# Performance work log

Hardware: AMD Instinct MI355X
Metric: run time of the kernel (lower is better)

## Reference

```python
import jax, jax.numpy as jnp
import numpy as np

N, D, L = 524288, 64, 20  # tokens, in_features, chain depth (20 Linear layers per branch)


def setup_inputs() -> dict:
    key = jax.random.key(0)
    kx, kw, kb = jax.random.split(key, 3)
    x = jax.random.normal(kx, (N, D), dtype=jnp.float32)
    # torch.nn.Linear default init: U(-1/sqrt(fan_in), 1/sqrt(fan_in))
    bound = 1.0 / np.sqrt(D)
    W = jax.random.uniform(kw, (L, D, D), dtype=jnp.float32, minval=-bound, maxval=bound)
    b = jax.random.uniform(kb, (L, D), dtype=jnp.float32, minval=-bound, maxval=bound)
    return {"x": x, "W": W, "b": b}


def reference(x, W, b):
    # is_hit=False => scatter routes ALL tokens to path 1 (path 0 is empty),
    # so forward = branches[1]: 20 sequential Linear(D, D) layers, then a
    # trivial gather (concat of the single non-empty branch result).
    # torch Linear: y = x @ W^T + b, W has shape [out, in].
    def step(h, wb):
        w, bias = wb  # w: [D, D], bias: [D]
        return h @ w.T + bias, None

    out, _ = jax.lax.scan(step, x, (W, b))
    return out
```

## Files before the change

kernel.cpp:

```cpp
#include <hip/hip_runtime.h>
#include <stdint.h>


using short8  = __attribute__((ext_vector_type(8))) short;
using floatx4 = __attribute__((ext_vector_type(4))) float;

#define N_TOK   524288
#define N_LAYER 20

#ifdef __has_builtin
#if __has_builtin(__builtin_amdgcn_cvt_pk_bf16_f32)
#define HAVE_CVT_PK_BF16 1
#endif
#endif

#ifdef HAVE_CVT_PK_BF16
typedef __bf16 bf16x2_t __attribute__((ext_vector_type(2)));
__device__ __forceinline__ uint32_t pk_bf16(float lo, float hi) {
  union { bf16x2_t v; uint32_t u; } c;
  c.v = __builtin_amdgcn_cvt_pk_bf16_f32(lo, hi);
  return c.u;
}
#else
__device__ __forceinline__ uint32_t pk_bf16(float lo, float hi) {
  uint32_t a = __float_as_uint(lo) + 0x8000u;
  uint32_t b = __float_as_uint(hi) + 0x8000u;
  return __builtin_amdgcn_perm(b, a, 0x07060302u);
}
#endif

__device__ __forceinline__ uint16_t bf16_rne(float f) {
  uint32_t u = __float_as_uint(f);
  u += 0x7fffu + ((u >> 16) & 1u);
  return (uint16_t)(u >> 16);
}

__global__ void prep_weights(const float* __restrict__ W, uint16_t* __restrict__ ws) {
  int idx  = blockIdx.x * 256 + threadIdx.x;
  int l    = idx >> 9;
  int rem  = idx & 511;
  int frag = rem >> 6;
  int lane = rem & 63;
  int mt = frag >> 1, ks = frag & 1;
  int m  = lane & 15;
  int q  = lane >> 4;
  int wrow = 32 * (mt >> 1) + 8 * (m >> 2) + 4 * (mt & 1) + (m & 3);
  int k0   = 32 * ks + 8 * q;
  const float* src = W + l * 4096 + wrow * 64 + k0;
  float4 f0 = *(const float4*)(src);
  float4 f1 = *(const float4*)(src + 4);
  union { uint16_t s[8]; uint4 v; } o;
  o.s[0] = bf16_rne(f0.x); o.s[1] = bf16_rne(f0.y);
  o.s[2] = bf16_rne(f0.z); o.s[3] = bf16_rne(f0.w);
  o.s[4] = bf16_rne(f1.x); o.s[5] = bf16_rne(f1.y);
  o.s[6] = bf16_rne(f1.z); o.s[7] = bf16_rne(f1.w);
  *(uint4*)(ws + (size_t)idx * 8) = o.v;
}

union BFrag { short8 v; uint32_t u[4]; };
union AFrag { short8 v; uint4 raw; };

__global__ __launch_bounds__(256, 3) void chain_fused(
    const float* __restrict__ x, const uint16_t* __restrict__ wf,
    const float* __restrict__ bias, float* __restrict__ out)
{
  __shared__ __align__(16) float biasLds[N_LAYER * 64];

  const int tid  = threadIdx.x;
  const int wv   = tid >> 6;
  const int lane = tid & 63;
  const int tl   = lane & 15;
  const int q    = lane >> 4;
  const int tokbase = blockIdx.x * 256 + wv * 64;

  for (int i = tid; i < N_LAYER * 64; i += 256) biasLds[i] = bias[i];

  BFrag Bf[4][2];
  #pragma unroll
  for (int tb = 0; tb < 4; tb++) {
    const float* xp = x + (size_t)(tokbase + tb * 16 + tl) * 64 + 8 * q;
    #pragma unroll
    for (int ks = 0; ks < 2; ks++) {
      float4 a0 = *(const float4*)(xp + 32 * ks);
      float4 a1 = *(const float4*)(xp + 32 * ks + 4);
      Bf[tb][ks].u[0] = pk_bf16(a0.x, a0.y);
      Bf[tb][ks].u[1] = pk_bf16(a0.z, a0.w);
      Bf[tb][ks].u[2] = pk_bf16(a1.x, a1.y);
      Bf[tb][ks].u[3] = pk_bf16(a1.z, a1.w);
    }
  }

  const uint4* wp = (const uint4*)wf;
  AFrag Af[8];
  #pragma unroll
  for (int f = 0; f < 8; f++) Af[f].raw = wp[f * 64 + lane];

  __syncthreads();

  floatx4 acc[4][4];
  #pragma unroll 2
  for (int l = 0; l < N_LAYER; l++) {
    const int ln = (l + 1 < N_LAYER) ? l + 1 : N_LAYER - 1;
    uint4 nf[8];
    #pragma unroll
    for (int f = 0; f < 8; f++) nf[f] = wp[(ln * 8 + f) * 64 + lane];

    #pragma unroll
    for (int mt = 0; mt < 4; mt++) {
      floatx4 bv = *(const floatx4*)(biasLds + l * 64 + 32 * (mt >> 1) + 4 * (mt & 1) + 8 * q);
      #pragma unroll
      for (int tb = 0; tb < 4; tb++) acc[tb][mt] = bv;
    }

    #pragma unroll
    for (int ks = 0; ks < 2; ks++)
      #pragma unroll
      for (int mt = 0; mt < 4; mt++)
        #pragma unroll
        for (int tb = 0; tb < 4; tb++)
          acc[tb][mt] = __builtin_amdgcn_mfma_f32_16x16x32_bf16(
              Af[mt * 2 + ks].v, Bf[tb][ks].v, acc[tb][mt], 0, 0, 0);

    if (l == N_LAYER - 1) break;

    #pragma unroll
    for (int tb = 0; tb < 4; tb++)
      #pragma unroll
      for (int mt = 0; mt < 4; mt++) {
        const int ksn = mt >> 1;
        const int d   = 2 * (mt & 1);
        Bf[tb][ksn].u[d]     = pk_bf16(acc[tb][mt][0], acc[tb][mt][1]);
        Bf[tb][ksn].u[d + 1] = pk_bf16(acc[tb][mt][2], acc[tb][mt][3]);
      }

    #pragma unroll
    for (int f = 0; f < 8; f++) Af[f].raw = nf[f];
  }

  #pragma unroll
  for (int tb = 0; tb < 4; tb++) {
    float* op = out + (size_t)(tokbase + tb * 16 + tl) * 64;
    #pragma unroll
    for (int mt = 0; mt < 4; mt++)
      *(floatx4*)(op + 32 * (mt >> 1) + 4 * (mt & 1) + 8 * q) = acc[tb][mt];
  }
}

extern "C" void kernel_launch(void* const* d_in, const int* in_sizes, int n_in,
                              void* d_out, int out_size, void* d_ws, size_t ws_size,
                              hipStream_t stream) {
  (void)in_sizes; (void)n_in; (void)out_size; (void)ws_size;
  const float* x = (const float*)d_in[0];
  const float* W = (const float*)d_in[1];
  const float* b = (const float*)d_in[2];
  float* out = (float*)d_out;
  uint16_t* ws = (uint16_t*)d_ws;

  prep_weights<<<dim3(40), dim3(256), 0, stream>>>(W, ws);
  chain_fused<<<dim3(N_TOK / 256), dim3(256), 0, stream>>>(x, ws, b, out);
}
```

Baseline: 277.8 us.

## Collapse 20-layer linear chain into a single composed affine map

```diff
diff --git a/kernel.cpp b/kernel.cpp
--- a/kernel.cpp
+++ b/kernel.cpp
@@ -7,6 +7,7 @@
 
 #define N_TOK   524288
 #define N_LAYER 20
+#define FPERM(mt, m) (32 * ((mt) >> 1) + 8 * ((m) >> 2) + 4 * ((mt) & 1) + ((m) & 3))
 
 #ifdef __has_builtin
 #if __has_builtin(__builtin_amdgcn_cvt_pk_bf16_f32)
@@ -29,43 +30,150 @@
 }
 #endif
 
+__device__ __forceinline__ float upk_lo(uint32_t p) { return __uint_as_float(p << 16); }
+__device__ __forceinline__ float upk_hi(uint32_t p) { return __uint_as_float(p & 0xffff0000u); }
+
 __device__ __forceinline__ uint16_t bf16_rne(float f) {
   uint32_t u = __float_as_uint(f);
   u += 0x7fffu + ((u >> 16) & 1u);
   return (uint16_t)(u >> 16);
 }
 
-__global__ void prep_weights(const float* __restrict__ W, uint16_t* __restrict__ ws) {
-  int idx  = blockIdx.x * 256 + threadIdx.x;
-  int l    = idx >> 9;
-  int rem  = idx & 511;
-  int frag = rem >> 6;
-  int lane = rem & 63;
-  int mt = frag >> 1, ks = frag & 1;
-  int m  = lane & 15;
-  int q  = lane >> 4;
-  int wrow = 32 * (mt >> 1) + 8 * (m >> 2) + 4 * (mt & 1) + (m & 3);
-  int k0   = 32 * ks + 8 * q;
-  const float* src = W + l * 4096 + wrow * 64 + k0;
-  float4 f0 = *(const float4*)(src);
-  float4 f1 = *(const float4*)(src + 4);
-  union { uint16_t s[8]; uint4 v; } o;
-  o.s[0] = bf16_rne(f0.x); o.s[1] = bf16_rne(f0.y);
-  o.s[2] = bf16_rne(f0.z); o.s[3] = bf16_rne(f0.w);
-  o.s[4] = bf16_rne(f1.x); o.s[5] = bf16_rne(f1.y);
-  o.s[6] = bf16_rne(f1.z); o.s[7] = bf16_rne(f1.w);
-  *(uint4*)(ws + (size_t)idx * 8) = o.v;
-}
-
 union BFrag { short8 v; uint32_t u[4]; };
-union AFrag { short8 v; uint4 raw; };
-
-__global__ __launch_bounds__(256, 3) void chain_fused(
-    const float* __restrict__ x, const uint16_t* __restrict__ wf,
-    const float* __restrict__ bias, float* __restrict__ out)
+union AFrag { short8 v; uint32_t u[4]; uint4 raw; };
+
+__global__ __launch_bounds__(128, 1) void compose(
+    const float* __restrict__ W, const float* __restrict__ bias,
+    uint16_t* __restrict__ afrag, float* __restrict__ vout)
 {
-  __shared__ __align__(16) float biasLds[N_LAYER * 64];
-
+  __shared__ float comp[65][64];
+
+  const int tid  = threadIdx.x;
+  const int twv  = tid >> 6;
+  const int lane = tid & 63;
+  const int tl   = lane & 15;
+  const int q    = lane >> 4;
+
+  BFrag Bh[4][2], Bl[4][2];
+  #pragma unroll
+  for (int tb = 0; tb < 4; tb++) {
+    const int tok = twv * 64 + tb * 16 + tl;
+    #pragma unroll
+    for (int ks = 0; ks < 2; ks++)
+      #pragma unroll
+      for (int p = 0; p < 4; p++) {
+        const int f0 = 32 * ks + 8 * q + 2 * p;
+        Bh[tb][ks].u[p] = pk_bf16(tok == f0 ? 1.0f : 0.0f, tok == f0 + 1 ? 1.0f : 0.0f);
+        Bl[tb][ks].u[p] = 0u;
+      }
+  }
+
+  floatx4 wr[2][8][2];
+  floatx4 br[2][4];
+
+  #define FETCH(L, buf)                                                          \
+    {                                                                            \
+      _Pragma("unroll") for (int mt = 0; mt < 4; mt++) {                         \
+        const int r = FPERM(mt, tl);                                             \
+        const float* base = W + (L) * 4096 + r * 64;                             \
+        _Pragma("unroll") for (int ks = 0; ks < 2; ks++) {                       \
+          wr[buf][mt * 2 + ks][0] = *(const floatx4*)(base + 32 * ks + 8 * q);   \
+          wr[buf][mt * 2 + ks][1] = *(const floatx4*)(base + 32 * ks + 8 * q + 4);\
+        }                                                                        \
+        br[buf][mt] = *(const floatx4*)(bias + (L) * 64 + 32 * (mt >> 1) + 4 * (mt & 1) + 8 * q); \
+      }                                                                          \
+    }
+
+  FETCH(0, 0);
+
+  floatx4 acc[4][4];
+  #pragma unroll 2
+  for (int l = 0; l < N_LAYER; l++) {
+    const int cur = l & 1;
+    if (l + 1 < N_LAYER) FETCH(l + 1, cur ^ 1);
+
+    AFrag Ah[8], Al[8];
+    #pragma unroll
+    for (int f = 0; f < 8; f++) {
+      #pragma unroll
+      for (int h = 0; h < 2; h++) {
+        floatx4 a = wr[cur][f][h];
+        uint32_t h0 = pk_bf16(a[0], a[1]);
+        uint32_t h1 = pk_bf16(a[2], a[3]);
+        Ah[f].u[2 * h]     = h0;
+        Ah[f].u[2 * h + 1] = h1;
+        Al[f].u[2 * h]     = pk_bf16(a[0] - upk_lo(h0), a[1] - upk_hi(h0));
+        Al[f].u[2 * h + 1] = pk_bf16(a[2] - upk_lo(h1), a[3] - upk_hi(h1));
+      }
+    }
+
+    #pragma unroll
+    for (int mt = 0; mt < 4; mt++)
+      #pragma unroll
+      for (int tb = 0; tb < 4; tb++) acc[tb][mt] = br[cur][mt];
+
+    #pragma unroll
+    for (int ks = 0; ks < 2; ks++)
+      #pragma unroll
+      for (int mt = 0; mt < 4; mt++) {
+        const int f = mt * 2 + ks;
+        #pragma unroll
+        for (int tb = 0; tb < 4; tb++) {
+          acc[tb][mt] = __builtin_amdgcn_mfma_f32_16x16x32_bf16(Ah[f].v, Bh[tb][ks].v, acc[tb][mt], 0, 0, 0);
+          acc[tb][mt] = __builtin_amdgcn_mfma_f32_16x16x32_bf16(Ah[f].v, Bl[tb][ks].v, acc[tb][mt], 0, 0, 0);
+          acc[tb][mt] = __builtin_amdgcn_mfma_f32_16x16x32_bf16(Al[f].v, Bh[tb][ks].v, acc[tb][mt], 0, 0, 0);
+        }
+      }
+
+    if (l == N_LAYER - 1) break;
+
+    #pragma unroll
+    for (int tb = 0; tb < 4; tb++)
+      #pragma unroll
+      for (int mt = 0; mt < 4; mt++) {
+        const int ksn = mt >> 1;
+        const int d   = 2 * (mt & 1);
+        uint32_t u0 = pk_bf16(acc[tb][mt][0], acc[tb][mt][1]);
+        uint32_t u1 = pk_bf16(acc[tb][mt][2], acc[tb][mt][3]);
+        Bh[tb][ksn].u[d]     = u0;
+        Bh[tb][ksn].u[d + 1] = u1;
+        Bl[tb][ksn].u[d]     = pk_bf16(acc[tb][mt][0] - upk_lo(u0), acc[tb][mt][1] - upk_hi(u0));
+        Bl[tb][ksn].u[d + 1] = pk_bf16(acc[tb][mt][2] - upk_lo(u1), acc[tb][mt][3] - upk_hi(u1));
+      }
+  }
+  #undef FETCH
+
+  if (twv == 0) {
+    #pragma unroll
+    for (int tb = 0; tb < 4; tb++)
+      #pragma unroll
+      for (int mt = 0; mt < 4; mt++)
+        *(floatx4*)&comp[tb * 16 + tl][32 * (mt >> 1) + 4 * (mt & 1) + 8 * q] = acc[tb][mt];
+  } else if (tl == 0) {
+    #pragma unroll
+    for (int mt = 0; mt < 4; mt++)
+      *(floatx4*)&comp[64][32 * (mt >> 1) + 4 * (mt & 1) + 8 * q] = acc[0][mt];
+  }
+  __syncthreads();
+
+  for (int it = tid; it < 512; it += 128) {
+    const int f  = it >> 6, ln = it & 63;
+    const int mt = f >> 1,  ks = f & 1;
+    const int m  = ln & 15, qq = ln >> 4;
+    const int r  = FPERM(mt, m);
+    const float vr = comp[64][r];
+    union { uint16_t s[8]; uint4 v; } o;
+    #pragma unroll
+    for (int j = 0; j < 8; j++) o.s[j] = bf16_rne(comp[32 * ks + 8 * qq + j][r] - vr);
+    *(uint4*)(afrag + (size_t)it * 8) = o.v;
+  }
+  if (tid < 64) vout[tid] = comp[64][tid];
+}
+
+__global__ __launch_bounds__(256, 3) void apply_affine(
+    const float* __restrict__ x, const uint16_t* __restrict__ afrag,
+    const float* __restrict__ vvec, float* __restrict__ out)
+{
   const int tid  = threadIdx.x;
   const int wv   = tid >> 6;
   const int lane = tid & 63;
@@ -73,7 +181,15 @@
   const int q    = lane >> 4;
   const int tokbase = blockIdx.x * 256 + wv * 64;
 
-  for (int i = tid; i < N_LAYER * 64; i += 256) biasLds[i] = bias[i];
+  const uint4* wp = (const uint4*)afrag;
+  AFrag Af[8];
+  #pragma unroll
+  for (int f = 0; f < 8; f++) Af[f].raw = wp[f * 64 + lane];
+
+  floatx4 bv[4];
+  #pragma unroll
+  for (int mt = 0; mt < 4; mt++)
+    bv[mt] = *(const floatx4*)(vvec + 32 * (mt >> 1) + 4 * (mt & 1) + 8 * q);
 
   BFrag Bf[4][2];
   #pragma unroll
@@ -81,61 +197,29 @@
     const float* xp = x + (size_t)(tokbase + tb * 16 + tl) * 64 + 8 * q;
     #pragma unroll
     for (int ks = 0; ks < 2; ks++) {
-      float4 a0 = *(const float4*)(xp + 32 * ks);
-      float4 a1 = *(const float4*)(xp + 32 * ks + 4);
-      Bf[tb][ks].u[0] = pk_bf16(a0.x, a0.y);
-      Bf[tb][ks].u[1] = pk_bf16(a0.z, a0.w);
-      Bf[tb][ks].u[2] = pk_bf16(a1.x, a1.y);
-      Bf[tb][ks].u[3] = pk_bf16(a1.z, a1.w);
+      floatx4 a0 = *(const floatx4*)(xp + 32 * ks);
+      floatx4 a1 = *(const floatx4*)(xp + 32 * ks + 4);
+      Bf[tb][ks].u[0] = pk_bf16(a0[0], a0[1]);
+      Bf[tb][ks].u[1] = pk_bf16(a0[2], a0[3]);
+      Bf[tb][ks].u[2] = pk_bf16(a1[0], a1[1]);
+      Bf[tb][ks].u[3] = pk_bf16(a1[2], a1[3]);
     }
   }
 
-  const uint4* wp = (const uint4*)wf;
-  AFrag Af[8];
-  #pragma unroll
-  for (int f = 0; f < 8; f++) Af[f].raw = wp[f * 64 + lane];
-
-  __syncthreads();
-
   floatx4 acc[4][4];
-  #pragma unroll 2
-  for (int l = 0; l < N_LAYER; l++) {
-    const int ln = (l + 1 < N_LAYER) ? l + 1 : N_LAYER - 1;
-    uint4 nf[8];
-    #pragma unroll
-    for (int f = 0; f < 8; f++) nf[f] = wp[(ln * 8 + f) * 64 + lane];
-
-    #pragma unroll
-    for (int mt = 0; mt < 4; mt++) {
-      floatx4 bv = *(const floatx4*)(biasLds + l * 64 + 32 * (mt >> 1) + 4 * (mt & 1) + 8 * q);
-      #pragma unroll
-      for (int tb = 0; tb < 4; tb++) acc[tb][mt] = bv;
-    }
-
-    #pragma unroll
-    for (int ks = 0; ks < 2; ks++)
-      #pragma unroll
-      for (int mt = 0; mt < 4; mt++)
-        #pragma unroll
-        for (int tb = 0; tb < 4; tb++)
-          acc[tb][mt] = __builtin_amdgcn_mfma_f32_16x16x32_bf16(
-              Af[mt * 2 + ks].v, Bf[tb][ks].v, acc[tb][mt], 0, 0, 0);
-
-    if (l == N_LAYER - 1) break;
-
-    #pragma unroll
-    for (int tb = 0; tb < 4; tb++)
-      #pragma unroll
-      for (int mt = 0; mt < 4; mt++) {
-        const int ksn = mt >> 1;
-        const int d   = 2 * (mt & 1);
-        Bf[tb][ksn].u[d]     = pk_bf16(acc[tb][mt][0], acc[tb][mt][1]);
-        Bf[tb][ksn].u[d + 1] = pk_bf16(acc[tb][mt][2], acc[tb][mt][3]);
-      }
-
-    #pragma unroll
-    for (int f = 0; f < 8; f++) Af[f].raw = nf[f];
-  }
+  #pragma unroll
+  for (int tb = 0; tb < 4; tb++)
+    #pragma unroll
+    for (int mt = 0; mt < 4; mt++) acc[tb][mt] = bv[mt];
+
+  #pragma unroll
+  for (int ks = 0; ks < 2; ks++)
+    #pragma unroll
+    for (int mt = 0; mt < 4; mt++)
+      #pragma unroll
+      for (int tb = 0; tb < 4; tb++)
+        acc[tb][mt] = __builtin_amdgcn_mfma_f32_16x16x32_bf16(
+            Af[mt * 2 + ks].v, Bf[tb][ks].v, acc[tb][mt], 0, 0, 0);
 
   #pragma unroll
   for (int tb = 0; tb < 4; tb++) {
@@ -154,8 +238,10 @@
   const float* W = (const float*)d_in[1];
   const float* b = (const float*)d_in[2];
   float* out = (float*)d_out;
-  uint16_t* ws = (uint16_t*)d_ws;
-
-  prep_weights<<<dim3(40), dim3(256), 0, stream>>>(W, ws);
-  chain_fused<<<dim3(N_TOK / 256), dim3(256), 0, stream>>>(x, ws, b, out);
-}
+
+  uint16_t* afrag = (uint16_t*)d_ws;
+  float*    vvec  = (float*)((char*)d_ws + 8192);
+
+  compose<<<dim3(1), dim3(128), 0, stream>>>(W, b, afrag, vvec);
+  apply_affine<<<dim3(N_TOK / 256), dim3(256), 0, stream>>>(x, afrag, vvec, out);
+}
```

Result: slower. 376.0 us (+35.3%).
